# Performance work log

Measured on AMD Instinct MI355X. Metric: run time of the kernel, lower is better.

The kernel has to match this reference:

```python
import jax, jax.numpy as jnp
import numpy as np

N_AGT, N_CTX, E, D, NC = 100000, 10000, 1000000, 128, 2


def _gn(x, w, b, eps=1e-5):
    # GroupNorm(num_groups=1) on (N, C): normalize over channels, affine.
    m = jnp.mean(x, axis=-1, keepdims=True)
    v = jnp.mean((x - m) ** 2, axis=-1, keepdims=True)
    return (x - m) * jax.lax.rsqrt(v + eps) * w + b


def setup_inputs() -> dict:
    key = jax.random.key(0)
    ks = jax.random.split(key, 16)
    s = 0.05  # weight scale
    return {
        "agts": jax.random.normal(ks[0], (N_AGT, D), jnp.float32),
        "ctx": jax.random.normal(ks[1], (N_CTX, D), jnp.float32),
        "agt_ctrs": jax.random.normal(ks[2], (N_AGT, NC), jnp.float32),
        "ctx_ctrs": jax.random.normal(ks[3], (N_CTX, NC), jnp.float32),
        "hi": jax.random.randint(ks[4], (E,), 0, N_AGT, jnp.int32),
        "wi": jax.random.randint(ks[5], (E,), 0, N_CTX, jnp.int32),
        "dist_w1": jax.random.normal(ks[6], (D, NC), jnp.float32) * s,
        "dist_b1": jnp.zeros((D,), jnp.float32),
        "dist_w2": jax.random.normal(ks[7], (D, D), jnp.float32) * s,
        "dist_gw": jnp.ones((D,), jnp.float32),
        "dist_gb": jnp.zeros((D,), jnp.float32),
        "q_w": jax.random.normal(ks[8], (D, D), jnp.float32) * s,
        "q_gw": jnp.ones((D,), jnp.float32),
        "q_gb": jnp.zeros((D,), jnp.float32),
        "ctx_w1": jax.random.normal(ks[9], (D, 3 * D), jnp.float32) * s,
        "ctx_gw": jnp.ones((D,), jnp.float32),
        "ctx_gb": jnp.zeros((D,), jnp.float32),
        "ctx_w2": jax.random.normal(ks[10], (D, D), jnp.float32) * s,
        "agt_w": jax.random.normal(ks[11], (D, D), jnp.float32) * s,
        "norm_gw": jnp.ones((D,), jnp.float32),
        "norm_gb": jnp.zeros((D,), jnp.float32),
        "lin_w": jax.random.normal(ks[12], (D, D), jnp.float32) * s,
        "lin_gw": jnp.ones((D,), jnp.float32),
        "lin_gb": jnp.zeros((D,), jnp.float32),
    }


def reference(agts, ctx, agt_ctrs, ctx_ctrs, hi, wi,
              dist_w1, dist_b1, dist_w2, dist_gw, dist_gb,
              q_w, q_gw, q_gb,
              ctx_w1, ctx_gw, ctx_gb, ctx_w2,
              agt_w, norm_gw, norm_gb,
              lin_w, lin_gw, lin_gb):
    res = agts
    # per-edge relative displacement: [E, 2]
    d = agt_ctrs[hi] - ctx_ctrs[wi]
    # dist MLP: Linear(2,128)+ReLU, Linear(128,128,nobias)+GN+ReLU
    d = jax.nn.relu(d @ dist_w1.T + dist_b1)
    d = jax.nn.relu(_gn(d @ dist_w2.T, dist_gw, dist_gb))
    # query: Linear(128,128,nobias)+GN+ReLU on gathered agents
    q = jax.nn.relu(_gn(agts[hi] @ q_w.T, q_gw, q_gb))
    # concat-MLP over edges: [E, 384] -> [E, 128]
    c = jnp.concatenate([d, q, ctx[wi]], axis=1)
    c = jax.nn.relu(_gn(c @ ctx_w1.T, ctx_gw, ctx_gb))
    c = c @ ctx_w2.T
    # agent transform + index_add scatter of edge messages
    a = agts @ agt_w.T
    a = a.at[hi].add(c)
    a = jax.nn.relu(_gn(a, norm_gw, norm_gb))
    a = _gn(a @ lin_w.T, lin_gw, lin_gb)  # Linear block with act=False
    a = jax.nn.relu(a + res)
    return a
```

## Files before the change

### kernel.cpp

```cpp
#include <hip/hip_runtime.h>
#include <stdint.h>


#define N_AGT 100000
#define N_CTX 10000
#define NE    1000000
#define D     128

typedef __attribute__((ext_vector_type(8))) __bf16 bf16x8;
typedef __attribute__((ext_vector_type(4))) float f32x4;
typedef __attribute__((ext_vector_type(4))) unsigned int uint32x4;
typedef __attribute__((ext_vector_type(8))) unsigned short ushort8;

__device__ __forceinline__ float bf_lo(uint32_t u){ return __uint_as_float(u << 16); }
__device__ __forceinline__ float bf_hi(uint32_t u){ return __uint_as_float(u & 0xFFFF0000u); }
__device__ __forceinline__ uint16_t f2bf(float f){
  uint32_t u = __float_as_uint(f);
  u += 0x7FFFu + ((u >> 16) & 1u);
  return (uint16_t)(u >> 16);
}
__device__ __forceinline__ float bf2f(uint16_t v){ return __uint_as_float(((uint32_t)v) << 16); }

__device__ __forceinline__ f32x4 mfma16(bf16x8 a, bf16x8 b, f32x4 c){
  return __builtin_amdgcn_mfma_f32_16x16x32_bf16(a, b, c, 0, 0, 0);
}

__device__ __forceinline__ void bar_lds(){
  asm volatile("s_waitcnt lgkmcnt(0)" ::: "memory");
  __builtin_amdgcn_s_barrier();
  __builtin_amdgcn_sched_barrier(0);
}


__device__ __forceinline__ void stage_wsz(char* dst, const float* __restrict__ W,
                                          int rs, int co, int tid, int nthr){
  for (int idx = tid; idx < 128*16; idx += nthr){
    const int row = idx >> 4, ch = idx & 15;
    const float4 f0 = *(const float4*)(W + (size_t)row*rs + co + ch*8);
    const float4 f1 = *(const float4*)(W + (size_t)row*rs + co + ch*8 + 4);
    ushort8 u;
    u[0]=f2bf(f0.x); u[1]=f2bf(f0.y); u[2]=f2bf(f0.z); u[3]=f2bf(f0.w);
    u[4]=f2bf(f1.x); u[5]=f2bf(f1.y); u[6]=f2bf(f1.z); u[7]=f2bf(f1.w);
    *(uint32x4*)(dst + row*256 + ((ch*16) ^ ((row&7)<<4))) = __builtin_bit_cast(uint32x4, u);
  }
}

__device__ __forceinline__ bf16x8 ldfrag(const char* base, int row, int cb){
  return __builtin_bit_cast(bf16x8,
      *(const uint32x4*)(base + row*256 + (cb ^ ((row&7)<<4))));
}

__device__ __forceinline__ void mm_stage(const char* xb, const char* wm, int wv,
                                         int llo, int lhi, f32x4 acc[3][2]){
  #pragma unroll
  for (int kt = 0; kt < 4; kt++){
    const int cb = kt*64 + lhi*16;
    const bf16x8 b0 = ldfrag(wm, wv*32 + llo,      cb);
    const bf16x8 b1 = ldfrag(wm, wv*32 + 16 + llo, cb);
    #pragma unroll
    for (int mt = 0; mt < 3; mt++){
      const bf16x8 a = ldfrag(xb, mt*16 + llo, cb);
      acc[mt][0] = mfma16(a, b0, acc[mt][0]);
      acc[mt][1] = mfma16(a, b1, acc[mt][1]);
    }
  }
}

__device__ __forceinline__ void scat_acc(char* xb, const f32x4 acc[3][2],
                                         int wv, int llo, int lhi){
  #pragma unroll
  for (int mt = 0; mt < 3; mt++)
    #pragma unroll
    for (int ntl = 0; ntl < 2; ntl++)
      #pragma unroll
      for (int r = 0; r < 4; r++){
        const int m = mt*16 + lhi*4 + r;
        const int n = wv*32 + ntl*16 + llo;
        *(uint16_t*)(xb + m*256 + ((n*2) ^ ((m&7)<<4))) = f2bf(acc[mt][ntl][r]);
      }
}

__device__ __forceinline__ void gn_rowpass(char* xb, const int rr[3], int llo,
                                           const float gw[8], const float gb[8]){
  #pragma unroll
  for (int i = 0; i < 3; i++){
    const int row = rr[i];
    char* p = xb + row*256 + ((llo*16) ^ ((row&7)<<4));
    ushort8 u = __builtin_bit_cast(ushort8, *(const uint32x4*)p);
    float f[8]; float s = 0.f, ss = 0.f;
    #pragma unroll
    for (int j = 0; j < 8; j++){ f[j] = bf2f(u[j]); s += f[j]; ss += f[j]*f[j]; }
    #pragma unroll
    for (int m = 1; m < 16; m <<= 1){ s += __shfl_xor(s, m); ss += __shfl_xor(ss, m); }
    const float mean = s*(1.f/128.f);
    const float var  = ss*(1.f/128.f) - mean*mean;
    const float rstd = rsqrtf(var + 1e-5f);
    #pragma unroll
    for (int j = 0; j < 8; j++){
      const float g = fmaxf((f[j]-mean)*rstd*gw[j] + gb[j], 0.f);
      u[j] = f2bf(g);
    }
    *(uint32x4*)p = __builtin_bit_cast(uint32x4, u);
  }
}

__device__ __forceinline__ void gn_rowpass_add(char* xb, const int rr[3], int llo,
                                               const float gw[8], const float gb[8],
                                               const ushort8 qs[3]){
  #pragma unroll
  for (int i = 0; i < 3; i++){
    const int row = rr[i];
    char* p = xb + row*256 + ((llo*16) ^ ((row&7)<<4));
    ushort8 u = __builtin_bit_cast(ushort8, *(const uint32x4*)p);
    float f[8]; float s = 0.f, ss = 0.f;
    #pragma unroll
    for (int j = 0; j < 8; j++){
      f[j] = bf2f(u[j]) + bf2f(qs[i][j]);
      s += f[j]; ss += f[j]*f[j];
    }
    #pragma unroll
    for (int m = 1; m < 16; m <<= 1){ s += __shfl_xor(s, m); ss += __shfl_xor(ss, m); }
    const float mean = s*(1.f/128.f);
    const float var  = ss*(1.f/128.f) - mean*mean;
    const float rstd = rsqrtf(var + 1e-5f);
    #pragma unroll
    for (int j = 0; j < 8; j++){
      const float g = fmaxf((f[j]-mean)*rstd*gw[j] + gb[j], 0.f);
      u[j] = f2bf(g);
    }
    *(uint32x4*)p = __builtin_bit_cast(uint32x4, u);
  }
}

#define GE      96
#define NITER_E ((NE + GE - 1) / GE)

__global__ __launch_bounds__(512, 2) void k_edge_mfma(
    const float* __restrict__ agt_ctrs, const float* __restrict__ ctx_ctrs,
    const int* __restrict__ hi, const int* __restrict__ wi,
    const float* __restrict__ dist_w1, const float* __restrict__ dist_b1,
    const float* __restrict__ dist_gw, const float* __restrict__ dist_gb,
    const float* __restrict__ ctx_gw, const float* __restrict__ ctx_gb,
    const float* __restrict__ dist_w2, const float* __restrict__ ctx_w1,
    const float* __restrict__ ctx_w2,
    const uint16_t* __restrict__ QW, const uint16_t* __restrict__ CtxP,
    float* __restrict__ A0){
  extern __shared__ __align__(16) char smem[];
  const int tid  = threadIdx.x;
  const int wave = tid >> 6, lane = tid & 63;
  const int grp  = wave >> 2, wv = wave & 3;
  const int lhi  = lane >> 4, llo = lane & 15;

  stage_wsz(smem,         dist_w2, 128, 0, tid, 512);
  stage_wsz(smem + 32768, ctx_w1,  384, 0, tid, 512);
  stage_wsz(smem + 65536, ctx_w2,  128, 0, tid, 512);

  char* xbA = smem + 98304 + grp*24576;
  char* xbB = xbA + 12288;
  int*  hb  = (int*)(smem + 147456) + grp*96;

  const int c0 = llo*8;
  float w1x[8], w1y[8], b1v[8], dgw[8], dgb[8], cgw[8], cgb[8];
  #pragma unroll
  for (int j = 0; j < 8; j++){
    w1x[j] = dist_w1[(c0+j)*2 + 0];
    w1y[j] = dist_w1[(c0+j)*2 + 1];
    b1v[j] = dist_b1[c0+j];
    dgw[j] = dist_gw[c0+j]; dgb[j] = dist_gb[c0+j];
    cgw[j] = ctx_gw[c0+j];  cgb[j] = ctx_gb[c0+j];
  }

  int rr[3];
  #pragma unroll
  for (int i = 0; i < 3; i++) rr[i] = wv*12 + i*4 + lhi;

  ushort8 qg[3], cg[3];
  float2 acs[3], ccs[3];

  const long step = gridDim.x;
  long it = blockIdx.x;
  if (it < NITER_E){
    const long ebase = it*GE + grp*48;
    #pragma unroll
    for (int i = 0; i < 3; i++){
      long e = ebase + rr[i]; if (e >= NE) e = NE - 1;
      const int h = hi[e], w = wi[e];
      qg[i]  = *(const ushort8*)&QW  [(size_t)h*D + c0];
      cg[i]  = *(const ushort8*)&CtxP[(size_t)w*D + c0];
      acs[i] = *(const float2*)&agt_ctrs[(size_t)h*2];
      ccs[i] = *(const float2*)&ctx_ctrs[(size_t)w*2];
    }
    if (wv == 0 && lane < 48){
      long e = ebase + lane; if (e >= NE) e = NE - 1;
      hb[lane] = hi[e];
    }
  }
  __syncthreads();

  int pb = 0;
  for (; it < NITER_E; it += step, pb ^= 1){
    const long ebase = it*GE + grp*48;
    ushort8 qs[3];
    #pragma unroll
    for (int i = 0; i < 3; i++){
      const float dx = acs[i].x - ccs[i].x, dy = acs[i].y - ccs[i].y;
      ushort8 u;
      #pragma unroll
      for (int j = 0; j < 8; j++)
        u[j] = f2bf(fmaxf(fmaf(dx, w1x[j], fmaf(dy, w1y[j], b1v[j])), 0.f));
      *(uint32x4*)(xbA + rr[i]*256 + ((llo*16) ^ ((rr[i]&7)<<4))) =
          __builtin_bit_cast(uint32x4, u);
      ushort8 v;
      #pragma unroll
      for (int j = 0; j < 8; j++) v[j] = f2bf(bf2f(qg[i][j]) + bf2f(cg[i][j]));
      qs[i] = v;
    }
    const long nit = it + step;
    if (nit < NITER_E){
      const long nbase = nit*GE + grp*48;
      #pragma unroll
      for (int i = 0; i < 3; i++){
        long e = nbase + rr[i]; if (e >= NE) e = NE - 1;
        const int h = hi[e], w = wi[e];
        qg[i]  = *(const ushort8*)&QW  [(size_t)h*D + c0];
        cg[i]  = *(const ushort8*)&CtxP[(size_t)w*D + c0];
        acs[i] = *(const float2*)&agt_ctrs[(size_t)h*2];
        ccs[i] = *(const float2*)&ctx_ctrs[(size_t)w*2];
      }
      if (wv == 0 && lane < 48){
        long e = nbase + lane; if (e >= NE) e = NE - 1;
        hb[(pb^1)*48 + lane] = hi[e];
      }
    }
    bar_lds();
    f32x4 acc1[3][2];
    #pragma unroll
    for (int mt = 0; mt < 3; mt++){ acc1[mt][0] = (f32x4)0.f; acc1[mt][1] = (f32x4)0.f; }
    mm_stage(xbA, smem, wv, llo, lhi, acc1);
    scat_acc(xbB, acc1, wv, llo, lhi);
    bar_lds();
    gn_rowpass(xbB, rr, llo, dgw, dgb);
    bar_lds();
    f32x4 acc2[3][2];
    #pragma unroll
    for (int mt = 0; mt < 3; mt++){ acc2[mt][0] = (f32x4)0.f; acc2[mt][1] = (f32x4)0.f; }
    mm_stage(xbB, smem + 32768, wv, llo, lhi, acc2);
    scat_acc(xbA, acc2, wv, llo, lhi);
    bar_lds();
    gn_rowpass_add(xbA, rr, llo, cgw, cgb, qs);
    bar_lds();
    f32x4 acc3[3][2];
    #pragma unroll
    for (int mt = 0; mt < 3; mt++){ acc3[mt][0] = (f32x4)0.f; acc3[mt][1] = (f32x4)0.f; }
    mm_stage(xbA, smem + 65536, wv, llo, lhi, acc3);
    #pragma unroll
    for (int mt = 0; mt < 3; mt++)
      #pragma unroll
      for (int ntl = 0; ntl < 2; ntl++)
        #pragma unroll
        for (int r = 0; r < 4; r++){
          const int m = mt*16 + lhi*4 + r;
          if (ebase + m < NE){
            const int n = wv*32 + ntl*16 + llo;
            atomicAdd(&A0[(size_t)hb[pb*48 + m]*D + n], acc3[mt][ntl][r]);
          }
        }
    bar_lds();
  }
}

#define NITER_A ((N_AGT + 95) / 96)

__global__ __launch_bounds__(512, 2) void k_agent_pre_mfma(
    const float* __restrict__ agts, const float* __restrict__ q_w,
    const float* __restrict__ ctx_w1, const float* __restrict__ agt_w,
    const float* __restrict__ q_gw, const float* __restrict__ q_gb,
    uint16_t* __restrict__ QW, float* __restrict__ A0){
  extern __shared__ __align__(16) char smem[];
  const int tid  = threadIdx.x;
  const int wave = tid >> 6, lane = tid & 63;
  const int grp  = wave >> 2, wv = wave & 3;
  const int lhi  = lane >> 4, llo = lane & 15;

  stage_wsz(smem,         q_w,    128, 0,   tid, 512);
  stage_wsz(smem + 32768, agt_w,  128, 0,   tid, 512);
  stage_wsz(smem + 65536, ctx_w1, 384, 128, tid, 512);

  char* xb = smem + 98304 + grp*12288;
  const int c0 = llo*8;
  float qgw[8], qgb[8];
  #pragma unroll
  for (int j = 0; j < 8; j++){ qgw[j] = q_gw[c0+j]; qgb[j] = q_gb[c0+j]; }
  __syncthreads();

  const int tg = tid & 255;
  int rr[3];
  #pragma unroll
  for (int i = 0; i < 3; i++) rr[i] = wv*12 + i*4 + lhi;

  for (int it = blockIdx.x; it < NITER_A; it += gridDim.x){
    const int rbase = it*96 + grp*48;
    for (int idx = tg; idx < 48*32; idx += 256){
      const int row = idx >> 5, c4 = idx & 31;
      int gr = rbase + row; if (gr >= N_AGT) gr = N_AGT - 1;
      const float4 f = *(const float4*)(agts + (size_t)gr*D + c4*4);
      const uint32_t lo = ((uint32_t)f2bf(f.y) << 16) | (uint32_t)f2bf(f.x);
      const uint32_t hi2 = ((uint32_t)f2bf(f.w) << 16) | (uint32_t)f2bf(f.z);
      *(uint2*)(xb + row*256 + ((c4*8) ^ ((row&7)<<4))) = make_uint2(lo, hi2);
    }
    __syncthreads();
    f32x4 acc[3][2];
    #pragma unroll
    for (int mt = 0; mt < 3; mt++){ acc[mt][0] = (f32x4)0.f; acc[mt][1] = (f32x4)0.f; }
    mm_stage(xb, smem + 32768, wv, llo, lhi, acc);
    #pragma unroll
    for (int mt = 0; mt < 3; mt++)
      #pragma unroll
      for (int ntl = 0; ntl < 2; ntl++)
        #pragma unroll
        for (int r = 0; r < 4; r++){
          const int m = mt*16 + lhi*4 + r;
          if (rbase + m < N_AGT){
            const int n = wv*32 + ntl*16 + llo;
            A0[(size_t)(rbase + m)*D + n] = acc[mt][ntl][r];
          }
        }
    #pragma unroll
    for (int mt = 0; mt < 3; mt++){ acc[mt][0] = (f32x4)0.f; acc[mt][1] = (f32x4)0.f; }
    mm_stage(xb, smem, wv, llo, lhi, acc);
    __syncthreads();
    scat_acc(xb, acc, wv, llo, lhi);
    __syncthreads();
    gn_rowpass(xb, rr, llo, qgw, qgb);
    __syncthreads();
    #pragma unroll
    for (int mt = 0; mt < 3; mt++){ acc[mt][0] = (f32x4)0.f; acc[mt][1] = (f32x4)0.f; }
    mm_stage(xb, smem + 65536, wv, llo, lhi, acc);
    __syncthreads();
    scat_acc(xb, acc, wv, llo, lhi);
    __syncthreads();
    #pragma unroll
    for (int i = 0; i < 3; i++){
      const int row = rr[i], gr = rbase + row;
      if (gr < N_AGT){
        const uint32x4 u = *(const uint32x4*)(xb + row*256 + ((llo*16) ^ ((row&7)<<4)));
        *(uint32x4*)(QW + (size_t)gr*D + c0) = u;
      }
    }
    __syncthreads();
  }
}

__global__ __launch_bounds__(512, 4) void k_post_mfma(
    float* __restrict__ A0, const float* __restrict__ agts,
    const float* __restrict__ lin_w,
    const float* __restrict__ norm_gw, const float* __restrict__ norm_gb,
    const float* __restrict__ lin_gw, const float* __restrict__ lin_gb){
  extern __shared__ __align__(16) char smem[];
  const int tid  = threadIdx.x;
  const int wave = tid >> 6, lane = tid & 63;
  const int grp  = wave >> 2, wv = wave & 3;
  const int lhi  = lane >> 4, llo = lane & 15;

  stage_wsz(smem, lin_w, 128, 0, tid, 512);
  char* xb = smem + 32768 + grp*12288;
  const int c0 = llo*8;
  float ngw[8], ngb[8], lgw[8], lgb[8];
  #pragma unroll
  for (int j = 0; j < 8; j++){
    ngw[j] = norm_gw[c0+j]; ngb[j] = norm_gb[c0+j];
    lgw[j] = lin_gw[c0+j];  lgb[j] = lin_gb[c0+j];
  }
  __syncthreads();

  int rr[3];
  #pragma unroll
  for (int i = 0; i < 3; i++) rr[i] = wv*12 + i*4 + lhi;

  for (int it = blockIdx.x; it < NITER_A; it += gridDim.x){
    const int rbase = it*96 + grp*48;
    #pragma unroll
    for (int i = 0; i < 3; i++){
      const int row = rr[i];
      int gr = rbase + row; if (gr >= N_AGT) gr = N_AGT - 1;
      const float4 a0 = *(const float4*)(A0 + (size_t)gr*D + c0);
      const float4 a1 = *(const float4*)(A0 + (size_t)gr*D + c0 + 4);
      float f[8] = {a0.x,a0.y,a0.z,a0.w,a1.x,a1.y,a1.z,a1.w};
      float s = 0.f, ss = 0.f;
      #pragma unroll
      for (int j = 0; j < 8; j++){ s += f[j]; ss += f[j]*f[j]; }
      #pragma unroll
      for (int m = 1; m < 16; m <<= 1){ s += __shfl_xor(s, m); ss += __shfl_xor(ss, m); }
      const float mean = s*(1.f/128.f);
      const float var  = ss*(1.f/128.f) - mean*mean;
      const float rstd = rsqrtf(var + 1e-5f);
      ushort8 u;
      #pragma unroll
      for (int j = 0; j < 8; j++)
        u[j] = f2bf(fmaxf((f[j]-mean)*rstd*ngw[j] + ngb[j], 0.f));
      *(uint32x4*)(xb + row*256 + ((llo*16) ^ ((row&7)<<4))) =
          __builtin_bit_cast(uint32x4, u);
    }
    __syncthreads();
    f32x4 acc[3][2];
    #pragma unroll
    for (int mt = 0; mt < 3; mt++){ acc[mt][0] = (f32x4)0.f; acc[mt][1] = (f32x4)0.f; }
    mm_stage(xb, smem, wv, llo, lhi, acc);
    __syncthreads();
    scat_acc(xb, acc, wv, llo, lhi);
    __syncthreads();
    #pragma unroll
    for (int i = 0; i < 3; i++){
      const int row = rr[i];
      const char* p = xb + row*256 + ((llo*16) ^ ((row&7)<<4));
      const ushort8 u = __builtin_bit_cast(ushort8, *(const uint32x4*)p);
      float f[8]; float s = 0.f, ss = 0.f;
      #pragma unroll
      for (int j = 0; j < 8; j++){ f[j] = bf2f(u[j]); s += f[j]; ss += f[j]*f[j]; }
      #pragma unroll
      for (int m = 1; m < 16; m <<= 1){ s += __shfl_xor(s, m); ss += __shfl_xor(ss, m); }
      const float mean = s*(1.f/128.f);
      const float var  = ss*(1.f/128.f) - mean*mean;
      const float rstd = rsqrtf(var + 1e-5f);
      const int gr = rbase + row;
      if (gr < N_AGT){
        const float4 r0 = *(const float4*)(agts + (size_t)gr*D + c0);
        const float4 r1 = *(const float4*)(agts + (size_t)gr*D + c0 + 4);
        const float res[8] = {r0.x,r0.y,r0.z,r0.w,r1.x,r1.y,r1.z,r1.w};
        float o[8];
        float4 o0, o1;
        #pragma unroll
        for (int j = 0; j < 8; j++)
          o[j] = fmaxf((f[j]-mean)*rstd*lgw[j] + lgb[j] + res[j], 0.f);
        o0.x=o[0]; o0.y=o[1]; o0.z=o[2]; o0.w=o[3];
        o1.x=o[4]; o1.y=o[5]; o1.z=o[6]; o1.w=o[7];
        *(float4*)(A0 + (size_t)gr*D + c0)     = o0;
        *(float4*)(A0 + (size_t)gr*D + c0 + 4) = o1;
      }
    }
    __syncthreads();
  }
}

__device__ __forceinline__ void stage_w4(uint32_t* wp, const float* __restrict__ W,
                                         int rs, int co, int tid, int nthr){
  for (int idx = tid; idx < 32*128; idx += nthr){
    int p2 = idx & 31, o = idx >> 5;
    const float4 f = *(const float4*)(W + (size_t)o*rs + co + p2*4);
    uint32_t lo = ((uint32_t)f2bf(f.y) << 16) | (uint32_t)f2bf(f.x);
    uint32_t hi = ((uint32_t)f2bf(f.w) << 16) | (uint32_t)f2bf(f.z);
    *(uint2*)&wp[(p2*128 + o)*2] = make_uint2(lo, hi);
  }
}

__device__ __forceinline__ float dot128(const uint32_t* wp, const float* xb, int o){
  float acc = 0.f;
  #pragma unroll 8
  for (int p2 = 0; p2 < 32; p2++){
    const uint2 w = *(const uint2*)&wp[(p2*128 + o)*2];
    const float4 x = *(const float4*)&xb[p2*4];
    acc += x.x*bf_lo(w.x) + x.y*bf_hi(w.x) + x.z*bf_lo(w.y) + x.w*bf_hi(w.y);
  }
  return acc;
}

__global__ __launch_bounds__(128) void k_ctx(const float* __restrict__ ctx,
                                             const float* __restrict__ ctx_w1,
                                             uint16_t* __restrict__ CtxP){
  __shared__ __align__(16) uint32_t wc[32*128*2];
  __shared__ __align__(16) float xbuf[128];
  const int tid = threadIdx.x;
  stage_w4(wc, ctx_w1, 384, 256, tid, 128);
  __syncthreads();
  for (int row = blockIdx.x; row < N_CTX; row += gridDim.x){
    __syncthreads();
    xbuf[tid] = ctx[(size_t)row*D + tid];
    __syncthreads();
    const float acc = dot128(wc, xbuf, tid);
    CtxP[(size_t)row*D + tid] = f2bf(acc);
  }
}

extern "C" void kernel_launch(void* const* d_in, const int* in_sizes, int n_in,
                              void* d_out, int out_size, void* d_ws, size_t ws_size,
                              hipStream_t stream){
  const float* agts     = (const float*)d_in[0];
  const float* ctx      = (const float*)d_in[1];
  const float* agt_ctrs = (const float*)d_in[2];
  const float* ctx_ctrs = (const float*)d_in[3];
  const int*   hi       = (const int*)d_in[4];
  const int*   wi       = (const int*)d_in[5];
  const float* dist_w1  = (const float*)d_in[6];
  const float* dist_b1  = (const float*)d_in[7];
  const float* dist_w2  = (const float*)d_in[8];
  const float* dist_gw  = (const float*)d_in[9];
  const float* dist_gb  = (const float*)d_in[10];
  const float* q_w      = (const float*)d_in[11];
  const float* q_gw     = (const float*)d_in[12];
  const float* q_gb     = (const float*)d_in[13];
  const float* ctx_w1   = (const float*)d_in[14];
  const float* ctx_gw   = (const float*)d_in[15];
  const float* ctx_gb   = (const float*)d_in[16];
  const float* ctx_w2   = (const float*)d_in[17];
  const float* agt_w    = (const float*)d_in[18];
  const float* norm_gw  = (const float*)d_in[19];
  const float* norm_gb  = (const float*)d_in[20];
  const float* lin_w    = (const float*)d_in[21];
  const float* lin_gw   = (const float*)d_in[22];
  const float* lin_gb   = (const float*)d_in[23];

  uint16_t* QW   = (uint16_t*)d_ws;
  uint16_t* CtxP = QW + (size_t)N_AGT * D;
  float*    A0   = (float*)d_out;

  const int EDGE_LDS = 148224;
  const int APRE_LDS = 122880;
  const int POST_LDS = 57344;
  hipFuncSetAttribute((const void*)k_edge_mfma,
                      hipFuncAttributeMaxDynamicSharedMemorySize, EDGE_LDS);
  hipFuncSetAttribute((const void*)k_agent_pre_mfma,
                      hipFuncAttributeMaxDynamicSharedMemorySize, APRE_LDS);
  hipFuncSetAttribute((const void*)k_post_mfma,
                      hipFuncAttributeMaxDynamicSharedMemorySize, POST_LDS);

  k_ctx<<<1024, 128, 0, stream>>>(ctx, ctx_w1, CtxP);
  k_agent_pre_mfma<<<256, 512, APRE_LDS, stream>>>(agts, q_w, ctx_w1, agt_w,
      q_gw, q_gb, QW, A0);
  k_edge_mfma<<<256, 512, EDGE_LDS, stream>>>(agt_ctrs, ctx_ctrs, hi, wi,
      dist_w1, dist_b1, dist_gw, dist_gb, ctx_gw, ctx_gb,
      dist_w2, ctx_w1, ctx_w2, QW, CtxP, A0);
  k_post_mfma<<<512, 512, POST_LDS, stream>>>(A0, agts, lin_w,
      norm_gw, norm_gb, lin_gw, lin_gb);
}
```

Baseline: 676.5 us.

## Restructure edge kernel to per-wave 16-edge tiles without block barriers

The edge kernel now gives each wave its own 16-edge tile and its own LDS scratch. Each wave computes all 128 output columns, so GroupNorm runs in registers with shuffle reductions instead of row passes through LDS. All block-level barriers are replaced by wave-local lgkmcnt waits, and the cross-iteration prefetch double-buffering of gathers is removed. In exchange, each wave rereads the whole weight matrix from LDS for every tile, the loads that overlapped the next iteration are gone, and it drops the NE tail guard (fine because NE is divisible by 16).

```diff
diff --git a/kernel.cpp b/kernel.cpp
--- a/kernel.cpp
+++ b/kernel.cpp
@@ -25,9 +25,8 @@
   return __builtin_amdgcn_mfma_f32_16x16x32_bf16(a, b, c, 0, 0, 0);
 }
 
-__device__ __forceinline__ void bar_lds(){
+__device__ __forceinline__ void wave_lgkm0(){
   asm volatile("s_waitcnt lgkmcnt(0)" ::: "memory");
-  __builtin_amdgcn_s_barrier();
   __builtin_amdgcn_sched_barrier(0);
 }
 
@@ -50,90 +49,66 @@
       *(const uint32x4*)(base + row*256 + (cb ^ ((row&7)<<4))));
 }
 
-__device__ __forceinline__ void mm_stage(const char* xb, const char* wm, int wv,
-                                         int llo, int lhi, f32x4 acc[3][2]){
-  #pragma unroll
-  for (int kt = 0; kt < 4; kt++){
-    const int cb = kt*64 + lhi*16;
-    const bf16x8 b0 = ldfrag(wm, wv*32 + llo,      cb);
-    const bf16x8 b1 = ldfrag(wm, wv*32 + 16 + llo, cb);
-    #pragma unroll
-    for (int mt = 0; mt < 3; mt++){
-      const bf16x8 a = ldfrag(xb, mt*16 + llo, cb);
-      acc[mt][0] = mfma16(a, b0, acc[mt][0]);
-      acc[mt][1] = mfma16(a, b1, acc[mt][1]);
-    }
-  }
-}
-
-__device__ __forceinline__ void scat_acc(char* xb, const f32x4 acc[3][2],
-                                         int wv, int llo, int lhi){
-  #pragma unroll
-  for (int mt = 0; mt < 3; mt++)
-    #pragma unroll
-    for (int ntl = 0; ntl < 2; ntl++)
-      #pragma unroll
-      for (int r = 0; r < 4; r++){
-        const int m = mt*16 + lhi*4 + r;
-        const int n = wv*32 + ntl*16 + llo;
-        *(uint16_t*)(xb + m*256 + ((n*2) ^ ((m&7)<<4))) = f2bf(acc[mt][ntl][r]);
-      }
-}
-
-__device__ __forceinline__ void gn_rowpass(char* xb, const int rr[3], int llo,
-                                           const float gw[8], const float gb[8]){
-  #pragma unroll
-  for (int i = 0; i < 3; i++){
-    const int row = rr[i];
-    char* p = xb + row*256 + ((llo*16) ^ ((row&7)<<4));
-    ushort8 u = __builtin_bit_cast(ushort8, *(const uint32x4*)p);
-    float f[8]; float s = 0.f, ss = 0.f;
-    #pragma unroll
-    for (int j = 0; j < 8; j++){ f[j] = bf2f(u[j]); s += f[j]; ss += f[j]*f[j]; }
-    #pragma unroll
-    for (int m = 1; m < 16; m <<= 1){ s += __shfl_xor(s, m); ss += __shfl_xor(ss, m); }
-    const float mean = s*(1.f/128.f);
-    const float var  = ss*(1.f/128.f) - mean*mean;
-    const float rstd = rsqrtf(var + 1e-5f);
-    #pragma unroll
-    for (int j = 0; j < 8; j++){
-      const float g = fmaxf((f[j]-mean)*rstd*gw[j] + gb[j], 0.f);
-      u[j] = f2bf(g);
-    }
-    *(uint32x4*)p = __builtin_bit_cast(uint32x4, u);
-  }
-}
-
-__device__ __forceinline__ void gn_rowpass_add(char* xb, const int rr[3], int llo,
-                                               const float gw[8], const float gb[8],
-                                               const ushort8 qs[3]){
-  #pragma unroll
-  for (int i = 0; i < 3; i++){
-    const int row = rr[i];
-    char* p = xb + row*256 + ((llo*16) ^ ((row&7)<<4));
-    ushort8 u = __builtin_bit_cast(ushort8, *(const uint32x4*)p);
-    float f[8]; float s = 0.f, ss = 0.f;
-    #pragma unroll
-    for (int j = 0; j < 8; j++){
-      f[j] = bf2f(u[j]) + bf2f(qs[i][j]);
-      s += f[j]; ss += f[j]*f[j];
-    }
-    #pragma unroll
-    for (int m = 1; m < 16; m <<= 1){ s += __shfl_xor(s, m); ss += __shfl_xor(ss, m); }
-    const float mean = s*(1.f/128.f);
-    const float var  = ss*(1.f/128.f) - mean*mean;
-    const float rstd = rsqrtf(var + 1e-5f);
-    #pragma unroll
-    for (int j = 0; j < 8; j++){
-      const float g = fmaxf((f[j]-mean)*rstd*gw[j] + gb[j], 0.f);
-      u[j] = f2bf(g);
-    }
-    *(uint32x4*)p = __builtin_bit_cast(uint32x4, u);
-  }
-}
-
-#define GE      96
-#define NITER_E ((NE + GE - 1) / GE)
+#define NWIT (NE/16)
+
+__device__ __forceinline__ void mm16(const char* T, const char* W,
+                                     int llo, int lhi, f32x4 acc[8]){
+  bf16x8 a[4];
+  #pragma unroll
+  for (int kt = 0; kt < 4; kt++) a[kt] = ldfrag(T, llo, kt*64 + lhi*16);
+  #pragma unroll
+  for (int nt = 0; nt < 8; nt++){
+    acc[nt] = (f32x4)0.f;
+    #pragma unroll
+    for (int kt = 0; kt < 4; kt++){
+      const bf16x8 b = ldfrag(W, nt*16 + llo, kt*64 + lhi*16);
+      acc[nt] = mfma16(a[kt], b, acc[nt]);
+    }
+  }
+}
+
+__device__ __forceinline__ void gn_reg(f32x4 acc[8], const float gw[8],
+                                       const float gb[8]){
+  float s[4] = {0,0,0,0}, ss[4] = {0,0,0,0};
+  #pragma unroll
+  for (int nt = 0; nt < 8; nt++)
+    #pragma unroll
+    for (int r = 0; r < 4; r++){
+      const float v = acc[nt][r];
+      s[r] += v; ss[r] += v*v;
+    }
+  #pragma unroll
+  for (int m = 1; m < 16; m <<= 1)
+    #pragma unroll
+    for (int r = 0; r < 4; r++){
+      s[r] += __shfl_xor(s[r], m);
+      ss[r] += __shfl_xor(ss[r], m);
+    }
+  float mean[4], rstd[4];
+  #pragma unroll
+  for (int r = 0; r < 4; r++){
+    mean[r] = s[r]*(1.f/128.f);
+    const float var = ss[r]*(1.f/128.f) - mean[r]*mean[r];
+    rstd[r] = rsqrtf(var + 1e-5f);
+  }
+  #pragma unroll
+  for (int nt = 0; nt < 8; nt++)
+    #pragma unroll
+    for (int r = 0; r < 4; r++)
+      acc[nt][r] = fmaxf((acc[nt][r]-mean[r])*rstd[r]*gw[nt] + gb[nt], 0.f);
+}
+
+__device__ __forceinline__ void scat16(char* T, const f32x4 acc[8],
+                                       int llo, int lhi){
+  #pragma unroll
+  for (int nt = 0; nt < 8; nt++)
+    #pragma unroll
+    for (int r = 0; r < 4; r++){
+      const int row = lhi*4 + r;
+      *(uint16_t*)(T + row*256 + ((2*(nt*16 + llo)) ^ ((row&7)<<4))) =
+          f2bf(acc[nt][r]);
+    }
+}
 
 __global__ __launch_bounds__(512, 2) void k_edge_mfma(
     const float* __restrict__ agt_ctrs, const float* __restrict__ ctx_ctrs,
@@ -148,124 +123,156 @@
   extern __shared__ __align__(16) char smem[];
   const int tid  = threadIdx.x;
   const int wave = tid >> 6, lane = tid & 63;
-  const int grp  = wave >> 2, wv = wave & 3;
   const int lhi  = lane >> 4, llo = lane & 15;
 
   stage_wsz(smem,         dist_w2, 128, 0, tid, 512);
   stage_wsz(smem + 32768, ctx_w1,  384, 0, tid, 512);
   stage_wsz(smem + 65536, ctx_w2,  128, 0, tid, 512);
 
-  char* xbA = smem + 98304 + grp*24576;
-  char* xbB = xbA + 12288;
-  int*  hb  = (int*)(smem + 147456) + grp*96;
+  char* T = smem + 98304 + wave*4096;
 
   const int c0 = llo*8;
-  float w1x[8], w1y[8], b1v[8], dgw[8], dgb[8], cgw[8], cgb[8];
+  float w1x[8], w1y[8], b1v[8];
   #pragma unroll
   for (int j = 0; j < 8; j++){
     w1x[j] = dist_w1[(c0+j)*2 + 0];
     w1y[j] = dist_w1[(c0+j)*2 + 1];
     b1v[j] = dist_b1[c0+j];
-    dgw[j] = dist_gw[c0+j]; dgb[j] = dist_gb[c0+j];
-    cgw[j] = ctx_gw[c0+j];  cgb[j] = ctx_gb[c0+j];
-  }
-
-  int rr[3];
-  #pragma unroll
-  for (int i = 0; i < 3; i++) rr[i] = wv*12 + i*4 + lhi;
-
-  ushort8 qg[3], cg[3];
-  float2 acs[3], ccs[3];
-
-  const long step = gridDim.x;
-  long it = blockIdx.x;
-  if (it < NITER_E){
-    const long ebase = it*GE + grp*48;
-    #pragma unroll
-    for (int i = 0; i < 3; i++){
-      long e = ebase + rr[i]; if (e >= NE) e = NE - 1;
-      const int h = hi[e], w = wi[e];
-      qg[i]  = *(const ushort8*)&QW  [(size_t)h*D + c0];
-      cg[i]  = *(const ushort8*)&CtxP[(size_t)w*D + c0];
-      acs[i] = *(const float2*)&agt_ctrs[(size_t)h*2];
-      ccs[i] = *(const float2*)&ctx_ctrs[(size_t)w*2];
-    }
-    if (wv == 0 && lane < 48){
-      long e = ebase + lane; if (e >= NE) e = NE - 1;
-      hb[lane] = hi[e];
-    }
+  }
+  float dgwr[8], dgbr[8], cgwr[8], cgbr[8];
+  #pragma unroll
+  for (int nt = 0; nt < 8; nt++){
+    dgwr[nt] = dist_gw[nt*16 + llo]; dgbr[nt] = dist_gb[nt*16 + llo];
+    cgwr[nt] = ctx_gw[nt*16 + llo];  cgbr[nt] = ctx_gb[nt*16 + llo];
   }
   __syncthreads();
 
-  int pb = 0;
-  for (; it < NITER_E; it += step, pb ^= 1){
-    const long ebase = it*GE + grp*48;
-    ushort8 qs[3];
-    #pragma unroll
-    for (int i = 0; i < 3; i++){
-      const float dx = acs[i].x - ccs[i].x, dy = acs[i].y - ccs[i].y;
+  const int wid = blockIdx.x*8 + wave;
+  const int nw  = gridDim.x*8;
+
+  for (int i = wid; i < NWIT; i += nw){
+    const int base = i*16;
+    const int4 h4 = *(const int4*)&hi[base + lhi*4];
+    const int4 w4 = *(const int4*)&wi[base + lhi*4];
+    const int hh[4] = {h4.x, h4.y, h4.z, h4.w};
+    const int ww[4] = {w4.x, w4.y, w4.z, w4.w};
+    const int h2 = hi[base + llo], w2 = wi[base + llo];
+    uint32x4 qql[4], qcl[4];
+    #pragma unroll
+    for (int k = 0; k < 4; k++){
+      qql[k] = *(const uint32x4*)&QW  [(size_t)h2*D + lhi*32 + k*8];
+      qcl[k] = *(const uint32x4*)&CtxP[(size_t)w2*D + lhi*32 + k*8];
+    }
+    #pragma unroll
+    for (int j = 0; j < 4; j++){
+      const float2 ac = *(const float2*)&agt_ctrs[(size_t)hh[j]*2];
+      const float2 cc = *(const float2*)&ctx_ctrs[(size_t)ww[j]*2];
+      const float dx = ac.x - cc.x, dy = ac.y - cc.y;
       ushort8 u;
       #pragma unroll
-      for (int j = 0; j < 8; j++)
-        u[j] = f2bf(fmaxf(fmaf(dx, w1x[j], fmaf(dy, w1y[j], b1v[j])), 0.f));
-      *(uint32x4*)(xbA + rr[i]*256 + ((llo*16) ^ ((rr[i]&7)<<4))) =
+      for (int c = 0; c < 8; c++)
+        u[c] = f2bf(fmaxf(fmaf(dx, w1x[c], fmaf(dy, w1y[c], b1v[c])), 0.f));
+      const int row = lhi*4 + j;
+      *(uint32x4*)(T + row*256 + ((llo*16) ^ ((row&7)<<4))) =
           __builtin_bit_cast(uint32x4, u);
+    }
+    wave_lgkm0();
+    f32x4 acc[8];
+    mm16(T, smem, llo, lhi, acc);
+    gn_reg(acc, dgwr, dgbr);
+    wave_lgkm0();
+    scat16(T, acc, llo, lhi);
+    wave_lgkm0();
+    mm16(T, smem + 32768, llo, lhi, acc);
+    ushort8 qs[4];
+    #pragma unroll
+    for (int k = 0; k < 4; k++){
+      const ushort8 a = __builtin_bit_cast(ushort8, qql[k]);
+      const ushort8 b = __builtin_bit_cast(ushort8, qcl[k]);
       ushort8 v;
       #pragma unroll
-      for (int j = 0; j < 8; j++) v[j] = f2bf(bf2f(qg[i][j]) + bf2f(cg[i][j]));
-      qs[i] = v;
-    }
-    const long nit = it + step;
-    if (nit < NITER_E){
-      const long nbase = nit*GE + grp*48;
-      #pragma unroll
-      for (int i = 0; i < 3; i++){
-        long e = nbase + rr[i]; if (e >= NE) e = NE - 1;
-        const int h = hi[e], w = wi[e];
-        qg[i]  = *(const ushort8*)&QW  [(size_t)h*D + c0];
-        cg[i]  = *(const ushort8*)&CtxP[(size_t)w*D + c0];
-        acs[i] = *(const float2*)&agt_ctrs[(size_t)h*2];
-        ccs[i] = *(const float2*)&ctx_ctrs[(size_t)w*2];
+      for (int j = 0; j < 8; j++) v[j] = f2bf(bf2f(a[j]) + bf2f(b[j]));
+      qs[k] = v;
+    }
+    wave_lgkm0();
+    #pragma unroll
+    for (int k = 0; k < 4; k++)
+      *(uint32x4*)(T + llo*256 + (((lhi*64) + k*16) ^ ((llo&7)<<4))) =
+          __builtin_bit_cast(uint32x4, qs[k]);
+    wave_lgkm0();
+    #pragma unroll
+    for (int nt = 0; nt < 8; nt++)
+      #pragma unroll
+      for (int r = 0; r < 4; r++){
+        const int row = lhi*4 + r;
+        const uint16_t q = *(const uint16_t*)(T + row*256 +
+            ((2*(nt*16 + llo)) ^ ((row&7)<<4)));
+        acc[nt][r] += bf2f(q);
       }
-      if (wv == 0 && lane < 48){
-        long e = nbase + lane; if (e >= NE) e = NE - 1;
-        hb[(pb^1)*48 + lane] = hi[e];
+    gn_reg(acc, cgwr, cgbr);
+    wave_lgkm0();
+    scat16(T, acc, llo, lhi);
+    wave_lgkm0();
+    mm16(T, smem + 65536, llo, lhi, acc);
+    #pragma unroll
+    for (int nt = 0; nt < 8; nt++)
+      #pragma unroll
+      for (int r = 0; r < 4; r++)
+        atomicAdd(&A0[(size_t)hh[r]*D + nt*16 + llo], acc[nt][r]);
+  }
+}
+
+__device__ __forceinline__ void mm_stage(const char* xb, const char* wm, int wv,
+                                         int llo, int lhi, f32x4 acc[3][2]){
+  #pragma unroll
+  for (int kt = 0; kt < 4; kt++){
+    const int cb = kt*64 + lhi*16;
+    const bf16x8 b0 = ldfrag(wm, wv*32 + llo,      cb);
+    const bf16x8 b1 = ldfrag(wm, wv*32 + 16 + llo, cb);
+    #pragma unroll
+    for (int mt = 0; mt < 3; mt++){
+      const bf16x8 a = ldfrag(xb, mt*16 + llo, cb);
+      acc[mt][0] = mfma16(a, b0, acc[mt][0]);
+      acc[mt][1] = mfma16(a, b1, acc[mt][1]);
+    }
+  }
+}
+
+__device__ __forceinline__ void scat_acc(char* xb, const f32x4 acc[3][2],
+                                         int wv, int llo, int lhi){
+  #pragma unroll
+  for (int mt = 0; mt < 3; mt++)
+    #pragma unroll
+    for (int ntl = 0; ntl < 2; ntl++)
+      #pragma unroll
+      for (int r = 0; r < 4; r++){
+        const int m = mt*16 + lhi*4 + r;
+        const int n = wv*32 + ntl*16 + llo;
+        *(uint16_t*)(xb + m*256 + ((n*2) ^ ((m&7)<<4))) = f2bf(acc[mt][ntl][r]);
       }
-    }
-    bar_lds();
-    f32x4 acc1[3][2];
-    #pragma unroll
-    for (int mt = 0; mt < 3; mt++){ acc1[mt][0] = (f32x4)0.f; acc1[mt][1] = (f32x4)0.f; }
-    mm_stage(xbA, smem, wv, llo, lhi, acc1);
-    scat_acc(xbB, acc1, wv, llo, lhi);
-    bar_lds();
-    gn_rowpass(xbB, rr, llo, dgw, dgb);
-    bar_lds();
-    f32x4 acc2[3][2];
-    #pragma unroll
-    for (int mt = 0; mt < 3; mt++){ acc2[mt][0] = (f32x4)0.f; acc2[mt][1] = (f32x4)0.f; }
-    mm_stage(xbB, smem + 32768, wv, llo, lhi, acc2);
-    scat_acc(xbA, acc2, wv, llo, lhi);
-    bar_lds();
-    gn_rowpass_add(xbA, rr, llo, cgw, cgb, qs);
-    bar_lds();
-    f32x4 acc3[3][2];
-    #pragma unroll
-    for (int mt = 0; mt < 3; mt++){ acc3[mt][0] = (f32x4)0.f; acc3[mt][1] = (f32x4)0.f; }
-    mm_stage(xbA, smem + 65536, wv, llo, lhi, acc3);
-    #pragma unroll
-    for (int mt = 0; mt < 3; mt++)
-      #pragma unroll
-      for (int ntl = 0; ntl < 2; ntl++)
-        #pragma unroll
-        for (int r = 0; r < 4; r++){
-          const int m = mt*16 + lhi*4 + r;
-          if (ebase + m < NE){
-            const int n = wv*32 + ntl*16 + llo;
-            atomicAdd(&A0[(size_t)hb[pb*48 + m]*D + n], acc3[mt][ntl][r]);
-          }
-        }
-    bar_lds();
+}
+
+__device__ __forceinline__ void gn_rowpass(char* xb, const int rr[3], int llo,
+                                           const float gw[8], const float gb[8]){
+  #pragma unroll
+  for (int i = 0; i < 3; i++){
+    const int row = rr[i];
+    char* p = xb + row*256 + ((llo*16) ^ ((row&7)<<4));
+    ushort8 u = __builtin_bit_cast(ushort8, *(const uint32x4*)p);
+    float f[8]; float s = 0.f, ss = 0.f;
+    #pragma unroll
+    for (int j = 0; j < 8; j++){ f[j] = bf2f(u[j]); s += f[j]; ss += f[j]*f[j]; }
+    #pragma unroll
+    for (int m = 1; m < 16; m <<= 1){ s += __shfl_xor(s, m); ss += __shfl_xor(ss, m); }
+    const float mean = s*(1.f/128.f);
+    const float var  = ss*(1.f/128.f) - mean*mean;
+    const float rstd = rsqrtf(var + 1e-5f);
+    #pragma unroll
+    for (int j = 0; j < 8; j++){
+      const float g = fmaxf((f[j]-mean)*rstd*gw[j] + gb[j], 0.f);
+      u[j] = f2bf(g);
+    }
+    *(uint32x4*)p = __builtin_bit_cast(uint32x4, u);
   }
 }
 
@@ -513,7 +520,7 @@
   uint16_t* CtxP = QW + (size_t)N_AGT * D;
   float*    A0   = (float*)d_out;
 
-  const int EDGE_LDS = 148224;
+  const int EDGE_LDS = 131072;
   const int APRE_LDS = 122880;
   const int POST_LDS = 57344;
   hipFuncSetAttribute((const void*)k_edge_mfma,
```

After: 614.1 us. 9.2% less time.
